# Kernel optimization log

Measured on AMD Instinct MI355X. Metric: run time of the kernel, lower is better.

The kernel has to match this reference:

```python
import jax, jax.numpy as jnp
import numpy as np

DIM = 4          # number of trunk networks (x, y, z, t)
H = 256          # hidden width for trunk and branch MLPs
R = 64           # CP rank
FD = 1           # field_dim
NF = 64          # Fourier feature half-width (B has shape (1, 64))
BRANCH_DIM = 256
DEPTH = 3        # MLP depth (3 hidden layers per eqx.nn.MLP semantics)


def _lin_init(key, out_dim, in_dim):
    return jax.random.normal(key, (out_dim, in_dim), dtype=jnp.float32) / jnp.sqrt(jnp.float32(in_dim))


def setup_inputs() -> dict:
    key = jax.random.key(0)
    ks = jax.random.split(key, 40)
    inp = {}
    # coordinate arrays, one per trunk: (N_i, 1)
    inp['x1'] = jax.random.uniform(ks[0], (64, 1), dtype=jnp.float32)
    inp['x2'] = jax.random.uniform(ks[1], (64, 1), dtype=jnp.float32)
    inp['x3'] = jax.random.uniform(ks[2], (64, 1), dtype=jnp.float32)
    inp['x4'] = jax.random.uniform(ks[3], (32, 1), dtype=jnp.float32)
    # branch input: batch of power maps, (B, branch_dim)
    inp['f'] = jax.random.normal(ks[4], (8, BRANCH_DIM), dtype=jnp.float32)
    # Fourier feature matrix B ~ 2*pi*N(0,1), shape (1, 64)
    inp['B'] = 2.0 * jnp.pi * jax.random.normal(ks[5], (1, NF), dtype=jnp.float32)
    # trunk ensemble params, stacked over the DIM trunks (all share shapes)
    inp['tW0'] = jnp.stack([_lin_init(ks[6 + i], H, 2 * NF) for i in range(DIM)])
    inp['tb0'] = jnp.zeros((DIM, H), dtype=jnp.float32)
    inp['tW1'] = jnp.stack([_lin_init(ks[10 + i], H, H) for i in range(DIM)])
    inp['tb1'] = jnp.zeros((DIM, H), dtype=jnp.float32)
    inp['tW2'] = jnp.stack([_lin_init(ks[14 + i], H, H) for i in range(DIM)])
    inp['tb2'] = jnp.zeros((DIM, H), dtype=jnp.float32)
    inp['tW3'] = jnp.stack([_lin_init(ks[18 + i], R * FD, H) for i in range(DIM)])
    inp['tb3'] = jnp.zeros((DIM, R * FD), dtype=jnp.float32)
    # branch MLP params
    inp['bW0'] = _lin_init(ks[30], H, BRANCH_DIM)
    inp['bb0'] = jnp.zeros((H,), dtype=jnp.float32)
    inp['bW1'] = _lin_init(ks[31], H, H)
    inp['bb1'] = jnp.zeros((H,), dtype=jnp.float32)
    inp['bW2'] = _lin_init(ks[32], H, H)
    inp['bb2'] = jnp.zeros((H,), dtype=jnp.float32)
    inp['bW3'] = _lin_init(ks[33], R * FD, H)
    inp['bb3'] = jnp.zeros((R * FD,), dtype=jnp.float32)
    return inp


def _forward(x1, x2, x3, x4, f, B,
             tW0, tb0, tW1, tb1, tW2, tb2, tW3, tb3,
             bW0, bb0, bW1, bb1, bW2, bb2, bW3, bb3):
    xs = [x1, x2, x3, x4]
    ts = []
    for i in range(DIM):
        p = xs[i] @ B                                  # (N_i, NF)
        feat = jnp.concatenate([jnp.cos(p), jnp.sin(p)], axis=1)  # (N_i, 2*NF)
        h = jax.nn.swish(feat @ tW0[i].T + tb0[i])
        h = jax.nn.swish(h @ tW1[i].T + tb1[i])
        h = jax.nn.swish(h @ tW2[i].T + tb2[i])
        t = (h @ tW3[i].T + tb3[i]).reshape(-1, FD, R)  # (N_i, y, z)
        ts.append(t)
    h = jax.nn.swish(f @ bW0.T + bb0)
    h = jax.nn.swish(h @ bW1.T + bb1)
    h = jax.nn.swish(h @ bW2.T + bb2)
    b = (h @ bW3.T + bb3).reshape(-1, FD, R)            # (B, y, z)
    # rank-R CP outer-product reconstruction: sum over z, shared field dim y
    return jnp.einsum('iyz,jyz,kyz,lyz,byz->bijkly',
                      ts[0], ts[1], ts[2], ts[3], b, optimize='optimal')


def reference(x1, x2, x3, x4, f, B,
              tW0, tb0, tW1, tb1, tW2, tb2, tW3, tb3,
              bW0, bb0, bW1, bb1, bW2, bb2, bW3, bb3):
    return _forward(x1, x2, x3, x4, f, B,
                    tW0, tb0, tW1, tb1, tW2, tb2, tW3, tb3,
                    bW0, bb0, bW1, bb1, bW2, bb2, bW3, bb3)
```

## Files before the change

### kernel.cpp

```cpp
#include <hip/hip_runtime.h>
#include <math.h>


#define HID 256
#define NFF 64

__global__ __launch_bounds__(256) void net_eval(
    const float* __restrict__ x1, const float* __restrict__ x2,
    const float* __restrict__ x3, const float* __restrict__ x4,
    const float* __restrict__ f,  const float* __restrict__ Bm,
    const float* __restrict__ tW0, const float* __restrict__ tb0,
    const float* __restrict__ tW1, const float* __restrict__ tb1,
    const float* __restrict__ tW2, const float* __restrict__ tb2,
    const float* __restrict__ tW3, const float* __restrict__ tb3,
    const float* __restrict__ bW0, const float* __restrict__ bb0,
    const float* __restrict__ bW1, const float* __restrict__ bb1,
    const float* __restrict__ bW2, const float* __restrict__ bb2,
    const float* __restrict__ bW3, const float* __restrict__ bb3,
    float* __restrict__ ws)
{
    __shared__ float bufA[HID];
    __shared__ float bufB[HID];
    const int t = threadIdx.x;
    const int bid = blockIdx.x;

    int net, row;
    if (bid < 192)      { net = bid >> 6; row = bid & 63; }
    else if (bid < 224) { net = 3;        row = bid - 192; }
    else                { net = 4;        row = bid - 224; }

    const float *W0, *B0v, *W1, *B1v, *W2, *B2v, *W3, *B3v;
    int in0;
    if (net < 4) {
        W0 = tW0 + (size_t)net * HID * 2 * NFF; B0v = tb0 + net * HID;
        W1 = tW1 + (size_t)net * HID * HID;     B1v = tb1 + net * HID;
        W2 = tW2 + (size_t)net * HID * HID;     B2v = tb2 + net * HID;
        W3 = tW3 + (size_t)net * 64 * HID;      B3v = tb3 + net * 64;
        in0 = 2 * NFF;
        const float* xp = (net == 0) ? x1 : (net == 1) ? x2 : (net == 2) ? x3 : x4;
        float xv = xp[row];
        if (t < 128) {
            float p = xv * Bm[t & 63];
            bufA[t] = (t < 64) ? cosf(p) : sinf(p);
        }
    } else {
        W0 = bW0; B0v = bb0; W1 = bW1; B1v = bb1;
        W2 = bW2; B2v = bb2; W3 = bW3; B3v = bb3;
        in0 = 256;
        bufA[t] = f[(size_t)row * 256 + t];
    }
    __syncthreads();

    {
        const float4* wr = (const float4*)(W0 + (size_t)t * in0);
        const float4* iv = (const float4*)bufA;
        const int n4 = in0 >> 2;
        float4 a4 = make_float4(0.f, 0.f, 0.f, 0.f);
        for (int k = 0; k < n4; ++k) {
            float4 w = wr[k]; float4 v = iv[k];
            a4.x += w.x * v.x; a4.y += w.y * v.y;
            a4.z += w.z * v.z; a4.w += w.w * v.w;
        }
        float acc = B0v[t] + ((a4.x + a4.y) + (a4.z + a4.w));
        bufB[t] = acc / (1.0f + expf(-acc));
    }
    __syncthreads();

    {
        const float4* wr = (const float4*)(W1 + (size_t)t * HID);
        const float4* iv = (const float4*)bufB;
        float4 a4 = make_float4(0.f, 0.f, 0.f, 0.f);
        for (int k = 0; k < HID / 4; ++k) {
            float4 w = wr[k]; float4 v = iv[k];
            a4.x += w.x * v.x; a4.y += w.y * v.y;
            a4.z += w.z * v.z; a4.w += w.w * v.w;
        }
        float acc = B1v[t] + ((a4.x + a4.y) + (a4.z + a4.w));
        bufA[t] = acc / (1.0f + expf(-acc));
    }
    __syncthreads();

    {
        const float4* wr = (const float4*)(W2 + (size_t)t * HID);
        const float4* iv = (const float4*)bufA;
        float4 a4 = make_float4(0.f, 0.f, 0.f, 0.f);
        for (int k = 0; k < HID / 4; ++k) {
            float4 w = wr[k]; float4 v = iv[k];
            a4.x += w.x * v.x; a4.y += w.y * v.y;
            a4.z += w.z * v.z; a4.w += w.w * v.w;
        }
        float acc = B2v[t] + ((a4.x + a4.y) + (a4.z + a4.w));
        bufB[t] = acc / (1.0f + expf(-acc));
    }
    __syncthreads();

    if (t < 64) {
        const float4* wr = (const float4*)(W3 + (size_t)t * HID);
        const float4* iv = (const float4*)bufB;
        float4 a4 = make_float4(0.f, 0.f, 0.f, 0.f);
        for (int k = 0; k < HID / 4; ++k) {
            float4 w = wr[k]; float4 v = iv[k];
            a4.x += w.x * v.x; a4.y += w.y * v.y;
            a4.z += w.z * v.z; a4.w += w.w * v.w;
        }
        float acc = B3v[t] + ((a4.x + a4.y) + (a4.z + a4.w));
        int base, stride;
        if      (net == 0) { base = 0;     stride = 64; }
        else if (net == 1) { base = 4096;  stride = 64; }
        else if (net == 2) { base = 8192;  stride = 64; }
        else if (net == 3) { base = 12288; stride = 32; }
        else               { base = 14336; stride = 8;  }
        ws[base + t * stride + row] = acc;
    }
}

__global__ __launch_bounds__(256) void cp_recon(
    const float* __restrict__ ws, float* __restrict__ out)
{
    __shared__ float t2s[64 * 64];
    __shared__ float t3s[64 * 32];
    __shared__ float sS[64 * 64];

    const int t = threadIdx.x;
    const int bid = blockIdx.x;
    const int b = bid >> 6;
    const int i = bid & 63;

    {
        const float4* ws4 = (const float4*)ws;
        float4* t2s4 = (float4*)t2s;
        float4* t3s4 = (float4*)t3s;
        #pragma unroll
        for (int m = 0; m < 4; ++m) t2s4[t + m * 256] = ws4[2048 + t + m * 256];
        #pragma unroll
        for (int m = 0; m < 2; ++m) t3s4[t + m * 256] = ws4[3072 + t + m * 256];
    }
    {
        const int j  = t & 63;
        const int zb = t >> 6;
        #pragma unroll
        for (int q = 0; q < 16; ++q) {
            int z = zb * 16 + q;
            sS[z * 64 + j] =
                ws[z * 64 + i] * ws[4096 + z * 64 + j] * ws[14336 + z * 8 + b];
        }
    }
    __syncthreads();

    const int jj   = t >> 6;
    const int lane = t & 63;
    const int k0   = (lane >> 3) * 8;
    const int l0   = (lane & 7) * 4;

    #pragma unroll 1
    for (int jt = 0; jt < 4; ++jt) {
        const int j0 = jt * 16;

        float4 acc[4][8];
        #pragma unroll
        for (int jl = 0; jl < 4; ++jl)
            #pragma unroll
            for (int kk = 0; kk < 8; ++kk)
                acc[jl][kk] = make_float4(0.f, 0.f, 0.f, 0.f);

        #pragma unroll 4
        for (int z = 0; z < 64; ++z) {
            float4 a0  = *(const float4*)&t2s[z * 64 + k0];
            float4 a1  = *(const float4*)&t2s[z * 64 + k0 + 4];
            float4 t3v = *(const float4*)&t3s[z * 32 + l0];
            float4 s4  = *(const float4*)&sS[z * 64 + j0 + jj * 4];
            const float ks0 = a0.x, ks1 = a0.y, ks2 = a0.z, ks3 = a0.w;
            const float ks4 = a1.x, ks5 = a1.y, ks6 = a1.z, ks7 = a1.w;
            #pragma unroll
            for (int jl = 0; jl < 4; ++jl) {
                const float sz = (jl == 0) ? s4.x : (jl == 1) ? s4.y
                               : (jl == 2) ? s4.z : s4.w;
                float4 u;
                u.x = sz * t3v.x; u.y = sz * t3v.y; u.z = sz * t3v.z; u.w = sz * t3v.w;
                acc[jl][0].x += ks0 * u.x; acc[jl][0].y += ks0 * u.y; acc[jl][0].z += ks0 * u.z; acc[jl][0].w += ks0 * u.w;
                acc[jl][1].x += ks1 * u.x; acc[jl][1].y += ks1 * u.y; acc[jl][1].z += ks1 * u.z; acc[jl][1].w += ks1 * u.w;
                acc[jl][2].x += ks2 * u.x; acc[jl][2].y += ks2 * u.y; acc[jl][2].z += ks2 * u.z; acc[jl][2].w += ks2 * u.w;
                acc[jl][3].x += ks3 * u.x; acc[jl][3].y += ks3 * u.y; acc[jl][3].z += ks3 * u.z; acc[jl][3].w += ks3 * u.w;
                acc[jl][4].x += ks4 * u.x; acc[jl][4].y += ks4 * u.y; acc[jl][4].z += ks4 * u.z; acc[jl][4].w += ks4 * u.w;
                acc[jl][5].x += ks5 * u.x; acc[jl][5].y += ks5 * u.y; acc[jl][5].z += ks5 * u.z; acc[jl][5].w += ks5 * u.w;
                acc[jl][6].x += ks6 * u.x; acc[jl][6].y += ks6 * u.y; acc[jl][6].z += ks6 * u.z; acc[jl][6].w += ks6 * u.w;
                acc[jl][7].x += ks7 * u.x; acc[jl][7].y += ks7 * u.y; acc[jl][7].z += ks7 * u.z; acc[jl][7].w += ks7 * u.w;
            }
        }

        #pragma unroll
        for (int jl = 0; jl < 4; ++jl) {
            const int j = j0 + jj * 4 + jl;
            size_t base = ((size_t)((b * 64 + i) * 64 + j)) * 2048;
            float* op = out + base;
            #pragma unroll
            for (int kk = 0; kk < 8; ++kk) {
                *(float4*)&op[(k0 + kk) * 32 + l0] = acc[jl][kk];
            }
        }
    }
}

extern "C" void kernel_launch(void* const* d_in, const int* in_sizes, int n_in,
                              void* d_out, int out_size, void* d_ws, size_t ws_size,
                              hipStream_t stream) {
    const float* x1  = (const float*)d_in[0];
    const float* x2  = (const float*)d_in[1];
    const float* x3  = (const float*)d_in[2];
    const float* x4  = (const float*)d_in[3];
    const float* f   = (const float*)d_in[4];
    const float* Bm  = (const float*)d_in[5];
    const float* tW0 = (const float*)d_in[6];
    const float* tb0 = (const float*)d_in[7];
    const float* tW1 = (const float*)d_in[8];
    const float* tb1 = (const float*)d_in[9];
    const float* tW2 = (const float*)d_in[10];
    const float* tb2 = (const float*)d_in[11];
    const float* tW3 = (const float*)d_in[12];
    const float* tb3 = (const float*)d_in[13];
    const float* bW0 = (const float*)d_in[14];
    const float* bb0 = (const float*)d_in[15];
    const float* bW1 = (const float*)d_in[16];
    const float* bb1 = (const float*)d_in[17];
    const float* bW2 = (const float*)d_in[18];
    const float* bb2 = (const float*)d_in[19];
    const float* bW3 = (const float*)d_in[20];
    const float* bb3 = (const float*)d_in[21];

    float* ws  = (float*)d_ws;
    float* out = (float*)d_out;

    hipLaunchKernelGGL(net_eval, dim3(232), dim3(256), 0, stream,
                       x1, x2, x3, x4, f, Bm,
                       tW0, tb0, tW1, tb1, tW2, tb2, tW3, tb3,
                       bW0, bb0, bW1, bb1, bW2, bb2, bW3, bb3, ws);
    hipLaunchKernelGGL(cp_recon, dim3(512), dim3(256), 0, stream, ws, out);
}
```

Measured before the change: 394.4 us.

## Rewrite CP reconstruction as split-bf16 MFMA GEMM over rank dimension

The CP outer-product reconstruction is recast as a GEMM. A is the S[j,z] matrix and B is the per-(k,l) product t2*t3 over z. The inner loop now runs on bf16 MFMA 16x16x32 instructions instead of scalar FP32 FMAs. Each operand is split into a bf16 high part and a bf16 residual, and three MFMAs per tile keep accuracy close to fp32. Shared-memory layouts are transposed and padded to suit MFMA fragment loads, at the cost of extra conversion work per element and output stores that are no longer float4 vectorised.

```diff
diff --git a/kernel.cpp b/kernel.cpp
--- a/kernel.cpp
+++ b/kernel.cpp
@@ -114,26 +114,42 @@
     }
 }
 
+
+#define PADZ 68
+#define PADS 72
+
+typedef __attribute__((ext_vector_type(8))) short bf16x8;
+typedef __attribute__((ext_vector_type(4))) float f32x4;
+
+__device__ __forceinline__ unsigned bf16_rne_bits(float x) {
+    unsigned u = __float_as_uint(x);
+    return (u + 0x7fffu + ((u >> 16) & 1u)) & 0xffff0000u;
+}
+
 __global__ __launch_bounds__(256) void cp_recon(
     const float* __restrict__ ws, float* __restrict__ out)
 {
-    __shared__ float t2s[64 * 64];
-    __shared__ float t3s[64 * 32];
-    __shared__ float sS[64 * 64];
+    __shared__ __attribute__((aligned(16))) float t2T2[64 * PADZ];
+    __shared__ __attribute__((aligned(16))) float t3T2[32 * PADZ];
+    __shared__ __attribute__((aligned(16))) unsigned short sHi [64 * PADS];
+    __shared__ __attribute__((aligned(16))) unsigned short sMid[64 * PADS];
 
     const int t = threadIdx.x;
     const int bid = blockIdx.x;
     const int b = bid >> 6;
     const int i = bid & 63;
 
-    {
-        const float4* ws4 = (const float4*)ws;
-        float4* t2s4 = (float4*)t2s;
-        float4* t3s4 = (float4*)t3s;
-        #pragma unroll
-        for (int m = 0; m < 4; ++m) t2s4[t + m * 256] = ws4[2048 + t + m * 256];
-        #pragma unroll
-        for (int m = 0; m < 2; ++m) t3s4[t + m * 256] = ws4[3072 + t + m * 256];
+    #pragma unroll
+    for (int m = 0; m < 16; ++m) {
+        int idx = t + m * 256;
+        int z = idx >> 6, k = idx & 63;
+        t2T2[k * PADZ + z] = ws[8192 + idx];
+    }
+    #pragma unroll
+    for (int m = 0; m < 8; ++m) {
+        int idx = t + m * 256;
+        int z = idx >> 5, lv = idx & 31;
+        t3T2[lv * PADZ + z] = ws[12288 + idx];
     }
     {
         const int j  = t & 63;
@@ -141,61 +157,84 @@
         #pragma unroll
         for (int q = 0; q < 16; ++q) {
             int z = zb * 16 + q;
-            sS[z * 64 + j] =
-                ws[z * 64 + i] * ws[4096 + z * 64 + j] * ws[14336 + z * 8 + b];
-        }
-    }
-    __syncthreads();
-
-    const int jj   = t >> 6;
+            float s = ws[z * 64 + i] * ws[4096 + z * 64 + j] * ws[14336 + z * 8 + b];
+            unsigned hb = bf16_rne_bits(s);
+            float r = s - __uint_as_float(hb);
+            sHi [j * PADS + z] = (unsigned short)(hb >> 16);
+            sMid[j * PADS + z] = (unsigned short)(__float_as_uint(r) >> 16);
+        }
+    }
+    __syncthreads();
+
+    const int w    = t >> 6;
     const int lane = t & 63;
-    const int k0   = (lane >> 3) * 8;
-    const int l0   = (lane & 7) * 4;
+    const int lg   = lane >> 4;
+    const int lr   = lane & 15;
+
+    bf16x8 Ah[4][2], Amid[4][2];
+    #pragma unroll
+    for (int m = 0; m < 4; ++m) {
+        #pragma unroll
+        for (int kt = 0; kt < 2; ++kt) {
+            int j = m * 16 + lr, z0 = kt * 32 + lg * 8;
+            Ah[m][kt]   = *(const bf16x8*)&sHi [j * PADS + z0];
+            Amid[m][kt] = *(const bf16x8*)&sMid[j * PADS + z0];
+        }
+    }
+    float t3r[2][2][8];
+    #pragma unroll
+    for (int par = 0; par < 2; ++par) {
+        #pragma unroll
+        for (int kt = 0; kt < 2; ++kt) {
+            const float* p = &t3T2[(par * 16 + lr) * PADZ + kt * 32 + lg * 8];
+            #pragma unroll
+            for (int e = 0; e < 8; ++e) t3r[par][kt][e] = p[e];
+        }
+    }
+
+    float* op = out + ((size_t)((b * 64 + i) * 64)) * 2048;
 
     #pragma unroll 1
-    for (int jt = 0; jt < 4; ++jt) {
-        const int j0 = jt * 16;
-
-        float4 acc[4][8];
-        #pragma unroll
-        for (int jl = 0; jl < 4; ++jl)
-            #pragma unroll
-            for (int kk = 0; kk < 8; ++kk)
-                acc[jl][kk] = make_float4(0.f, 0.f, 0.f, 0.f);
-
-        #pragma unroll 4
-        for (int z = 0; z < 64; ++z) {
-            float4 a0  = *(const float4*)&t2s[z * 64 + k0];
-            float4 a1  = *(const float4*)&t2s[z * 64 + k0 + 4];
-            float4 t3v = *(const float4*)&t3s[z * 32 + l0];
-            float4 s4  = *(const float4*)&sS[z * 64 + j0 + jj * 4];
-            const float ks0 = a0.x, ks1 = a0.y, ks2 = a0.z, ks3 = a0.w;
-            const float ks4 = a1.x, ks5 = a1.y, ks6 = a1.z, ks7 = a1.w;
-            #pragma unroll
-            for (int jl = 0; jl < 4; ++jl) {
-                const float sz = (jl == 0) ? s4.x : (jl == 1) ? s4.y
-                               : (jl == 2) ? s4.z : s4.w;
-                float4 u;
-                u.x = sz * t3v.x; u.y = sz * t3v.y; u.z = sz * t3v.z; u.w = sz * t3v.w;
-                acc[jl][0].x += ks0 * u.x; acc[jl][0].y += ks0 * u.y; acc[jl][0].z += ks0 * u.z; acc[jl][0].w += ks0 * u.w;
-                acc[jl][1].x += ks1 * u.x; acc[jl][1].y += ks1 * u.y; acc[jl][1].z += ks1 * u.z; acc[jl][1].w += ks1 * u.w;
-                acc[jl][2].x += ks2 * u.x; acc[jl][2].y += ks2 * u.y; acc[jl][2].z += ks2 * u.z; acc[jl][2].w += ks2 * u.w;
-                acc[jl][3].x += ks3 * u.x; acc[jl][3].y += ks3 * u.y; acc[jl][3].z += ks3 * u.z; acc[jl][3].w += ks3 * u.w;
-                acc[jl][4].x += ks4 * u.x; acc[jl][4].y += ks4 * u.y; acc[jl][4].z += ks4 * u.z; acc[jl][4].w += ks4 * u.w;
-                acc[jl][5].x += ks5 * u.x; acc[jl][5].y += ks5 * u.y; acc[jl][5].z += ks5 * u.z; acc[jl][5].w += ks5 * u.w;
-                acc[jl][6].x += ks6 * u.x; acc[jl][6].y += ks6 * u.y; acc[jl][6].z += ks6 * u.z; acc[jl][6].w += ks6 * u.w;
-                acc[jl][7].x += ks7 * u.x; acc[jl][7].y += ks7 * u.y; acc[jl][7].z += ks7 * u.z; acc[jl][7].w += ks7 * u.w;
+    for (int nn = 0; nn < 16; ++nn) {
+        const int n0 = w * 32 + nn * 2;
+        const int kcol = n0 >> 1;
+        float t2v[2][8];
+        #pragma unroll
+        for (int kt = 0; kt < 2; ++kt) {
+            const float* p = &t2T2[kcol * PADZ + kt * 32 + lg * 8];
+            #pragma unroll
+            for (int e = 0; e < 8; ++e) t2v[kt][e] = p[e];
+        }
+        #pragma unroll
+        for (int par = 0; par < 2; ++par) {
+            const int n = n0 + par;
+            bf16x8 Bh[2], Bm[2];
+            #pragma unroll
+            for (int kt = 0; kt < 2; ++kt) {
+                #pragma unroll
+                for (int e = 0; e < 8; ++e) {
+                    float pz = t2v[kt][e] * t3r[par][kt][e];
+                    unsigned hb = bf16_rne_bits(pz);
+                    float r = pz - __uint_as_float(hb);
+                    Bh[kt][e] = (short)(hb >> 16);
+                    Bm[kt][e] = (short)(__float_as_uint(r) >> 16);
+                }
             }
-        }
-
-        #pragma unroll
-        for (int jl = 0; jl < 4; ++jl) {
-            const int j = j0 + jj * 4 + jl;
-            size_t base = ((size_t)((b * 64 + i) * 64 + j)) * 2048;
-            float* op = out + base;
-            #pragma unroll
-            for (int kk = 0; kk < 8; ++kk) {
-                *(float4*)&op[(k0 + kk) * 32 + l0] = acc[jl][kk];
+            const int col = n * 16 + lr;
+            #pragma unroll
+            for (int m = 0; m < 4; ++m) {
+                f32x4 acc = {0.f, 0.f, 0.f, 0.f};
+                #pragma unroll
+                for (int kt = 0; kt < 2; ++kt) {
+                    acc = __builtin_amdgcn_mfma_f32_16x16x32_bf16(Ah[m][kt],   Bh[kt], acc, 0, 0, 0);
+                    acc = __builtin_amdgcn_mfma_f32_16x16x32_bf16(Amid[m][kt], Bh[kt], acc, 0, 0, 0);
+                    acc = __builtin_amdgcn_mfma_f32_16x16x32_bf16(Ah[m][kt],   Bm[kt], acc, 0, 0, 0);
+                }
+                const int jrow = m * 16 + lg * 4;
+                #pragma unroll
+                for (int r = 0; r < 4; ++r) {
+                    op[(size_t)(jrow + r) * 2048 + col] = acc[r];
+                }
             }
         }
     }
```

New measurement: 362.1 us. 1.09x faster.
